# Performance work log

Hardware: AMD Instinct MI355X
Metric: run time of the kernel (lower is better)

Reference implementation:

```python
import jax, jax.numpy as jnp
import numpy as np

N, LAT, H, R, L = 384, 64, 128, 16, 3
CUTOFF = 12.0
COORD_INIT_SCALE = 0.001


def setup_inputs() -> dict:
    key = jax.random.key(0)
    ks = jax.random.split(key, 12)
    def w(k, shape, fan):
        return jax.random.normal(k, shape, jnp.float32) / np.float32(np.sqrt(fan))
    return {
        "z": jax.random.normal(ks[0], (N, LAT), jnp.float32),
        # spread anchors so the radius graph is non-trivially sparse
        "anchor_coords": jax.random.normal(ks[1], (N, 3), jnp.float32) * 10.0,
        "proj_W": w(ks[2], (LAT, H), LAT),
        "proj_b": jnp.zeros((H,), jnp.float32),
        "eW1": w(ks[3], (L, 2 * H + R, H), 2 * H + R),
        "eb1": jnp.zeros((L, H), jnp.float32),
        "eW2": w(ks[4], (L, H, H), H),
        "eb2": jnp.zeros((L, H), jnp.float32),
        "nW1": w(ks[5], (L, 2 * H, H), 2 * H),
        "nb1": jnp.zeros((L, H), jnp.float32),
        "nW2": w(ks[6], (L, H, H), H),
        "nb2": jnp.zeros((L, H), jnp.float32),
        "cW1": w(ks[7], (L, H, H), H),
        "cb1": jnp.zeros((L, H), jnp.float32),
        # coord head scaled by coord_update_init_scale for stable coordinate updates
        "cW2": w(ks[8], (L, H, 1), H) * COORD_INIT_SCALE,
    }


def _rbf(d):
    # Gaussian radial basis expansion over [0, cutoff]
    mu = jnp.linspace(0.0, CUTOFF, R, dtype=d.dtype)            # (R,)
    gamma = jnp.asarray((R / CUTOFF) ** 2, d.dtype)
    return jnp.exp(-gamma * (d[..., None] - mu) ** 2)           # (..., R)


def reference(z, anchor_coords, proj_W, proj_b, eW1, eb1, eW2, eb2,
              nW1, nb1, nW2, nb2, cW1, cb1, cW2):
    silu = jax.nn.silu
    n = z.shape[0]
    h = z @ proj_W + proj_b                                      # (N, H)
    x = anchor_coords - anchor_coords.mean(0, keepdims=True)     # (N, 3)

    idx = jnp.arange(n)
    seq_mask = jnp.abs(idx[:, None] - idx[None, :]) == 1         # sequential edges
    eye = jnp.eye(n, dtype=bool)

    for l in range(L):
        # rebuild radius graph from current coords (dense jit-safe mask)
        diff = x[:, None, :] - x[None, :, :]                     # (N, N, 3) x_i - x_j
        d2 = jnp.sum(diff * diff, axis=-1)                       # (N, N)
        mask = ((d2 < CUTOFF ** 2) & ~eye) | seq_mask            # (N, N) bool
        maskf = mask.astype(h.dtype)
        d = jnp.sqrt(jnp.where(mask, d2, 1.0)) * maskf           # NaN-safe sqrt
        e = _rbf(d)                                              # (N, N, R)

        hi = jnp.broadcast_to(h[:, None, :], (n, n, H))          # receiver
        hj = jnp.broadcast_to(h[None, :, :], (n, n, H))          # sender
        m = silu(jnp.concatenate([hi, hj, e], -1) @ eW1[l] + eb1[l])
        m = silu(m @ eW2[l] + eb2[l]) * maskf[..., None]         # (N, N, H) messages

        agg = m.sum(1)                                           # scatter-add at receiver
        h = h + silu(jnp.concatenate([h, agg], -1) @ nW1[l] + nb1[l]) @ nW2[l] + nb2[l]

        w = (silu(m @ cW1[l] + cb1[l]) @ cW2[l]) * maskf[..., None]  # (N, N, 1)
        x = x + jnp.sum(diff * w, axis=1)                        # equivariant coord update
    return x
```

## Files before the change

### kernel.cpp

```cpp
#include <hip/hip_runtime.h>
#include <hip/hip_bf16.h>

#define NN 384
#define CUTOFF2 144.0f
#define GAMMA 1.7777778f

#define PK_L 26624
#define PK_WE 8192
#define PK_W2 10240
#define PK_C1 18432

#define STG_F32 1152
#define SCRATCH_B (8*STG_F32*4)
#define PERSIST_OFF (PK_L*4 + SCRATCH_B)
#define K_SMEM (PERSIST_OFF + 15408)

#define O_H    9216
#define O_A    205824
#define O_XA   0
#define O_XB   4608
#define O_HBF0 599040
#define O_HBF1 697344
#define O_MEAN 3076112
#define O_PK   3076160

typedef __bf16 bf16x8 __attribute__((ext_vector_type(8)));
typedef float f32x4 __attribute__((ext_vector_type(4)));

union ER { struct { float dx, dy, dz; unsigned j; } e; uint4 u4; };

__device__ __forceinline__ unsigned short f2bf(float f){
  unsigned u = __float_as_uint(f);
  return (unsigned short)((u + 0x7fffu + ((u >> 16) & 1u)) >> 16);
}
__device__ __forceinline__ unsigned pk2(float a, float b){
  return ((unsigned)f2bf(b) << 16) | f2bf(a);
}
__device__ __forceinline__ float silu(float x){ return x / (1.0f + __expf(-x)); }

__device__ __forceinline__ void scan_rows(
    int row, int rowsel, int t256, bool v, const float* __restrict__ x,
    uint4* sEr, int* pCnt){
  int* scnt = &pCnt[rowsel];
  if (t256 == 0) *scnt = 0;
  __syncthreads();
  if (v) {
    float xi0 = x[row*3], xi1 = x[row*3+1], xi2 = x[row*3+2];
    for (int j = t256; j < 384; j += 256) {
      float d0 = xi0-x[j*3], d1 = xi1-x[j*3+1], d2 = xi2-x[j*3+2];
      float dd = d0*d0 + d1*d1 + d2*d2;
      bool msk = ((dd < CUTOFF2) && (j != row)) || (j == row-1) || (j == row+1);
      if (msk) {
        int ss = atomicAdd(scnt, 1);
        ER er; er.e.dx = d0; er.e.dy = d1; er.e.dz = d2; er.e.j = (unsigned)j;
        sEr[rowsel*384 + ss] = er.u4;
      }
    }
  }
  __syncthreads();
  if (v) {
    int cnt = *scnt;
    int p = (32 - (cnt & 31)) & 31;
    if (t256 < p) {
      ER er; er.e.dx = 0.f; er.e.dy = 0.f; er.e.dz = 0.f; er.e.j = (unsigned)row;
      sEr[rowsel*384 + cnt + t256] = er.u4;
    }
  }
}

#define TRANSFORM(VA, VB, FA, FB)                                              \
  _Pragma("unroll")                                                            \
  for (int c = 0; c < 4; ++c) {                                                \
    _Pragma("unroll")                                                          \
    for (int tl = 0; tl < 2; ++tl) {                                           \
      int t = 2*c + tl;                                                        \
      _Pragma("unroll")                                                        \
      for (int r = 0; r < 4; ++r) {                                            \
        stg[(quad*4 + r)*36 + tl*16 + col0] = VA[t][r];                        \
        stg[(16 + quad*4 + r)*36 + tl*16 + col0] = VB[t][r];                   \
      }                                                                        \
    }                                                                          \
    float4 lo = *(const float4*)(stg + col0*36 + quad*8);                      \
    float4 hi = *(const float4*)(stg + col0*36 + quad*8 + 4);                  \
    FA[c].u = make_uint4(pk2(lo.x,lo.y), pk2(lo.z,lo.w),                       \
                         pk2(hi.x,hi.y), pk2(hi.z,hi.w));                      \
    float4 lo2 = *(const float4*)(stg + (16 + col0)*36 + quad*8);              \
    float4 hi2 = *(const float4*)(stg + (16 + col0)*36 + quad*8 + 4);          \
    FB[c].u = make_uint4(pk2(lo2.x,lo2.y), pk2(lo2.z,lo2.w),                   \
                         pk2(hi2.x,hi2.y), pk2(hi2.z,hi2.w));                  \
  }

__device__ __forceinline__ void edge_phase(
    const unsigned short* __restrict__ hbf,
    const unsigned* smem, float* scratch,
    const float* pSa, float* pSg, float* pDx, const int* pCnt, const uint4* sEr,
    const float* __restrict__ eb2g, const float* __restrict__ cb1g,
    const float* __restrict__ cw2g, int valid1){
  const int tid = threadIdx.x, q = tid & 63, s = tid >> 6;
  const int col0 = q & 15, quad = q >> 4;
  float eb2v[8], cb1v[8], cw2v[8];
  #pragma unroll
  for (int t = 0; t < 8; ++t) {
    int c = t*16 + col0;
    eb2v[t] = eb2g[c]; cb1v[t] = cb1g[c]; cw2v[t] = cw2g[c];
  }
  float* stg = scratch + s*STG_F32;
  const f32x4 z4 = {0.f, 0.f, 0.f, 0.f};
  union U8 { uint4 u; bf16x8 v; };

  const int nu0 = (pCnt[0] + 31) >> 5;
  const int nu1 = valid1 ? ((pCnt[1] + 31) >> 5) : 0;
  const int nu = nu0 + nu1;

  for (int k = s; k < nu; k += 8) {
    const int rs = (k < nu0) ? 0 : 1;
    const int ub = (k < nu0) ? k : k - nu0;
    int nvalid = pCnt[rs] - ub*32; if (nvalid > 32) nvalid = 32;
    float Aval[8];
    #pragma unroll
    for (int t = 0; t < 8; ++t) Aval[t] = pSa[rs*128 + t*16 + col0];
    ER e0, e1;
    e0.u4 = sEr[rs*384 + ub*32 + col0];
    e1.u4 = sEr[rs*384 + ub*32 + 16 + col0];
    const int j0 = (int)e0.e.j, j1 = (int)e1.e.j;
    const float d0x = e0.e.dx, d0y = e0.e.dy, d0z = e0.e.dz;
    const float d1x = e1.e.dx, d1y = e1.e.dy, d1z = e1.e.dz;
    const float dd0 = sqrtf(d0x*d0x + d0y*d0y + d0z*d0z);
    const float dd1 = sqrtf(d1x*d1x + d1y*d1y + d1z*d1z);

    U8 ha0[4], ha1[4];
    #pragma unroll
    for (int c = 0; c < 4; ++c) {
      ha0[c].u = *(const uint4*)(hbf + j0*128 + c*32 + quad*8);
      ha1[c].u = *(const uint4*)(hbf + j1*128 + c*32 + quad*8);
    }

    U8 cve0, cve1;
    if (q < 32) {
      #pragma unroll
      for (int tp = 0; tp < 4; ++tp) {
        float k0 = (float)(quad*8 + 2*tp);
        float t00 = dd0 - 0.8f*k0, t01 = dd0 - 0.8f*(k0+1.f);
        float t10 = dd1 - 0.8f*k0, t11 = dd1 - 0.8f*(k0+1.f);
        (&cve0.u.x)[tp] = pk2(__expf(-GAMMA*t00*t00), __expf(-GAMMA*t01*t01));
        (&cve1.u.x)[tp] = pk2(__expf(-GAMMA*t10*t10), __expf(-GAMMA*t11*t11));
      }
    } else { cve0.u = make_uint4(0,0,0,0); cve1.u = make_uint4(0,0,0,0); }

    f32x4 acc0[8], acc1[8];
    #pragma unroll
    for (int t = 0; t < 8; ++t) { acc0[t] = z4; acc1[t] = z4; }
    #pragma unroll
    for (int t = 0; t < 8; ++t) {
      #pragma unroll
      for (int c = 0; c < 4; ++c) {
        bf16x8 w = *(const bf16x8*)(smem + ((t*4 + c)*64 + q)*4);
        acc0[t] = __builtin_amdgcn_mfma_f32_16x16x32_bf16(ha0[c].v, w, acc0[t], 0, 0, 0);
        acc1[t] = __builtin_amdgcn_mfma_f32_16x16x32_bf16(ha1[c].v, w, acc1[t], 0, 0, 0);
      }
      bf16x8 we = *(const bf16x8*)(smem + PK_WE + (t*64 + q)*4);
      acc0[t] = __builtin_amdgcn_mfma_f32_16x16x32_bf16(cve0.v, we, acc0[t], 0, 0, 0);
      acc1[t] = __builtin_amdgcn_mfma_f32_16x16x32_bf16(cve1.v, we, acc1[t], 0, 0, 0);
    }
    #pragma unroll
    for (int t = 0; t < 8; ++t)
      #pragma unroll
      for (int r = 0; r < 4; ++r) {
        acc0[t][r] = silu(acc0[t][r] + Aval[t]);
        acc1[t][r] = silu(acc1[t][r] + Aval[t]);
      }

    U8 a20[4], a21[4];
    TRANSFORM(acc0, acc1, a20, a21);

    f32x4 m0[8], m1v[8];
    #pragma unroll
    for (int t = 0; t < 8; ++t) { m0[t] = z4; m1v[t] = z4; }
    #pragma unroll
    for (int t = 0; t < 8; ++t)
      #pragma unroll
      for (int c = 0; c < 4; ++c) {
        bf16x8 w = *(const bf16x8*)(smem + PK_W2 + ((t*4 + c)*64 + q)*4);
        m0[t] = __builtin_amdgcn_mfma_f32_16x16x32_bf16(a20[c].v, w, m0[t], 0, 0, 0);
        m1v[t] = __builtin_amdgcn_mfma_f32_16x16x32_bf16(a21[c].v, w, m1v[t], 0, 0, 0);
      }
    #pragma unroll
    for (int t = 0; t < 8; ++t) {
      float cs = 0.f;
      #pragma unroll
      for (int r = 0; r < 4; ++r) {
        m0[t][r] = silu(m0[t][r] + eb2v[t]);
        m1v[t][r] = silu(m1v[t][r] + eb2v[t]);
        if (quad*4 + r < nvalid) cs += m0[t][r];
        if (16 + quad*4 + r < nvalid) cs += m1v[t][r];
      }
      cs += __shfl_xor(cs, 16); cs += __shfl_xor(cs, 32);
      if (q < 16) atomicAdd(&pSg[rs*128 + t*16 + q], cs);
    }

    U8 a30[4], a31[4];
    TRANSFORM(m0, m1v, a30, a31);

    f32x4 c30[8], c31[8];
    #pragma unroll
    for (int t = 0; t < 8; ++t) { c30[t] = z4; c31[t] = z4; }
    #pragma unroll
    for (int t = 0; t < 8; ++t)
      #pragma unroll
      for (int c = 0; c < 4; ++c) {
        bf16x8 w = *(const bf16x8*)(smem + PK_C1 + ((t*4 + c)*64 + q)*4);
        c30[t] = __builtin_amdgcn_mfma_f32_16x16x32_bf16(a30[c].v, w, c30[t], 0, 0, 0);
        c31[t] = __builtin_amdgcn_mfma_f32_16x16x32_bf16(a31[c].v, w, c31[t], 0, 0, 0);
      }
    float p0[4], p1[4];
    #pragma unroll
    for (int r = 0; r < 4; ++r) {
      float pa = 0.f, pb = 0.f;
      #pragma unroll
      for (int t = 0; t < 8; ++t) {
        pa += silu(c30[t][r] + cb1v[t]) * cw2v[t];
        pb += silu(c31[t][r] + cb1v[t]) * cw2v[t];
      }
      if (quad*4 + r >= nvalid) pa = 0.f;
      if (16 + quad*4 + r >= nvalid) pb = 0.f;
      p0[r] = pa; p1[r] = pb;
    }
    #pragma unroll
    for (int r = 0; r < 4; ++r)
      #pragma unroll
      for (int off = 1; off < 16; off <<= 1) {
        p0[r] += __shfl_xor(p0[r], off);
        p1[r] += __shfl_xor(p1[r], off);
      }
    float dx0 = 0.f, dx1 = 0.f, dx2 = 0.f;
    #pragma unroll
    for (int r = 0; r < 4; ++r) {
      int el = quad*4 + r;
      float s0 = __shfl(d0x, el), s1 = __shfl(d0y, el), s2 = __shfl(d0z, el);
      if (col0 == 0) { dx0 += p0[r]*s0; dx1 += p0[r]*s1; dx2 += p0[r]*s2; }
      float u0 = __shfl(d1x, el), u1 = __shfl(d1y, el), u2 = __shfl(d1z, el);
      if (col0 == 0) { dx0 += p1[r]*u0; dx1 += p1[r]*u1; dx2 += p1[r]*u2; }
    }
    dx0 += __shfl_xor(dx0, 16); dx0 += __shfl_xor(dx0, 32);
    dx1 += __shfl_xor(dx1, 16); dx1 += __shfl_xor(dx1, 32);
    dx2 += __shfl_xor(dx2, 16); dx2 += __shfl_xor(dx2, 32);
    if (q == 0) {
      atomicAdd(&pDx[rs*4 + 0], dx0);
      atomicAdd(&pDx[rs*4 + 1], dx1);
      atomicAdd(&pDx[rs*4 + 2], dx2);
    }
  }
}

__device__ __forceinline__ void node_phase(
    const float* __restrict__ nW1l, const float* __restrict__ nb1l,
    const float* __restrict__ nW2l, const float* __restrict__ nb2l,
    const float* __restrict__ eW1n, const float* __restrict__ eb1n,
    unsigned short* __restrict__ hbf_out,
    float* __restrict__ hg, float* __restrict__ Ag,
    float* pSh, float* pSa, const float* pSg,
    float* scratch, int rowsel, int half, int o, int row, bool v){
  float* sb = scratch + rowsel*768;
  float* st = sb; float* part = sb + 128;

  float aa = 0.f;
  if (v) {
    const float* src = half ? (pSg + rowsel*128) : (pSh + rowsel*128);
    const float* wb  = nW1l + half*128*128;
    float a0=0,a1=0,a2=0,a3=0;
    #pragma unroll 16
    for (int k = 0; k < 128; k += 4) {
      a0 += src[k]   * wb[k*128 + o];
      a1 += src[k+1] * wb[(k+1)*128 + o];
      a2 += src[k+2] * wb[(k+2)*128 + o];
      a3 += src[k+3] * wb[(k+3)*128 + o];
    }
    aa = (a0+a1)+(a2+a3);
    if (half) part[o] = aa;
  }
  __syncthreads();
  if (v && !half) st[o] = silu(nb1l[o] + aa + part[o]);
  __syncthreads();
  float bb = 0.f;
  if (v) {
    int k0 = half*64;
    float b0=0,b1=0,b2=0,b3=0;
    #pragma unroll 16
    for (int k = k0; k < k0+64; k += 4) {
      b0 += st[k]   * nW2l[k*128 + o];
      b1 += st[k+1] * nW2l[(k+1)*128 + o];
      b2 += st[k+2] * nW2l[(k+2)*128 + o];
      b3 += st[k+3] * nW2l[(k+3)*128 + o];
    }
    bb = (b0+b1)+(b2+b3);
    if (half) part[o] = bb;
  }
  __syncthreads();
  if (v && !half) {
    float hn = pSh[rowsel*128 + o] + nb2l[o] + bb + part[o];
    pSh[rowsel*128 + o] = hn;
    hg[row*128 + o] = hn;
    hbf_out[row*128 + o] = f2bf(hn);
  }
  __syncthreads();
  float cc = 0.f;
  if (v) {
    const float* shn = pSh + rowsel*128;
    int k0 = half*64;
    float c0=0,c1=0,c2=0,c3=0;
    #pragma unroll 16
    for (int k = k0; k < k0+64; k += 4) {
      c0 += shn[k]   * eW1n[k*128 + o];
      c1 += shn[k+1] * eW1n[(k+1)*128 + o];
      c2 += shn[k+2] * eW1n[(k+2)*128 + o];
      c3 += shn[k+3] * eW1n[(k+3)*128 + o];
    }
    cc = (c0+c1)+(c2+c3);
    if (half) part[o] = cc;
  }
  __syncthreads();
  if (v && !half) Ag[row*128 + o] = eb1n[o] + cc + part[o];
}

__global__ __launch_bounds__(512) void k_init(
    const float* __restrict__ eW1, const float* __restrict__ eW2,
    const float* __restrict__ cW1, unsigned* __restrict__ pk,
    const float* __restrict__ anchor, const float* __restrict__ z,
    const float* __restrict__ pW, const float* __restrict__ pbias,
    const float* __restrict__ eb1, float* __restrict__ h,
    unsigned short* __restrict__ hbf, float* __restrict__ A,
    float* __restrict__ meanw){
  __shared__ float sb2[2*768];
  __shared__ float ssum[3];
  const int b = blockIdx.x, tid = threadIdx.x;
  const int rowsel = tid >> 8, half = (tid >> 7) & 1, o = tid & 127;
  {
    int t = b*512 + tid;
    if (t < 3*PK_L) {
      int layer = t / PK_L, r = t % PK_L;
      const float* src; int fr; int isWe = 0;
      if (r < PK_WE)        { fr = r;          src = eW1 + (layer*272 + 128)*128; }
      else if (r < PK_W2)   { fr = r - PK_WE;  src = eW1 + (layer*272 + 256)*128; isWe = 1; }
      else if (r < PK_C1)   { fr = r - PK_W2;  src = eW2 + layer*128*128; }
      else                  { fr = r - PK_C1;  src = cW1 + layer*128*128; }
      int tp = fr & 3, ll = (fr >> 2) & 63, nc = fr >> 8;
      int n, k;
      if (!isWe) { n = nc >> 2; int c = nc & 3; k = c*32 + ((ll>>4)<<3) + 2*tp; }
      else       { n = nc;                      k = ((ll>>4)<<3) + 2*tp; }
      int nn2 = n*16 + (ll & 15);
      float w0, w1;
      if (isWe) { w0 = (k < 16)   ? src[k*128+nn2]     : 0.f;
                  w1 = (k+1 < 16) ? src[(k+1)*128+nn2] : 0.f; }
      else      { w0 = src[k*128+nn2]; w1 = src[(k+1)*128+nn2]; }
      pk[t] = ((unsigned)f2bf(w1) << 16) | f2bf(w0);
    }
  }
  if (b == 0) {
    if (tid < 3) ssum[tid] = 0.f;
    __syncthreads();
    if (tid < 384) {
      atomicAdd(&ssum[0], anchor[tid*3]);
      atomicAdd(&ssum[1], anchor[tid*3+1]);
      atomicAdd(&ssum[2], anchor[tid*3+2]);
    }
    __syncthreads();
    if (tid < 3) meanw[tid] = ssum[tid]*(1.f/384.f);
  }
  const int row = b + 256*rowsel;
  const bool v = row < NN;
  float* sb = sb2 + rowsel*768;
  float* sh = sb; float* part = sb + 512; float* sz = sb + 640;
  if (v && half == 0 && o < 64) sz[o] = z[row*64 + o];
  __syncthreads();
  float pp = 0.f;
  if (v) {
    int k0 = half*32;
    float p0=0,p1=0,p2=0,p3=0;
    #pragma unroll 8
    for (int k = k0; k < k0+32; k += 4) {
      p0 += sz[k]   * pW[k*128 + o];
      p1 += sz[k+1] * pW[(k+1)*128 + o];
      p2 += sz[k+2] * pW[(k+2)*128 + o];
      p3 += sz[k+3] * pW[(k+3)*128 + o];
    }
    pp = (p0+p1)+(p2+p3);
    if (half) part[o] = pp;
  }
  __syncthreads();
  if (v && !half) {
    float hh = pbias[o] + pp + part[o];
    h[row*128 + o] = hh; sh[o] = hh;
    hbf[row*128 + o] = f2bf(hh);
  }
  __syncthreads();
  float cc = 0.f;
  if (v) {
    int k0 = half*64;
    float c0=0,c1=0,c2=0,c3=0;
    #pragma unroll 16
    for (int k = k0; k < k0+64; k += 4) {
      c0 += sh[k]   * eW1[k*128 + o];
      c1 += sh[k+1] * eW1[(k+1)*128 + o];
      c2 += sh[k+2] * eW1[(k+2)*128 + o];
      c3 += sh[k+3] * eW1[(k+3)*128 + o];
    }
    cc = (c0+c1)+(c2+c3);
    if (half) part[o] = cc;
  }
  __syncthreads();
  if (v && !half) A[row*128 + o] = eb1[o] + cc + part[o];
}

__global__ __launch_bounds__(512, 1) void k_layer(
    const unsigned* __restrict__ pkl,
    const float* __restrict__ x_src, float* __restrict__ x_dst,
    const unsigned short* __restrict__ hbf_in, unsigned short* __restrict__ hbf_out,
    float* __restrict__ h, float* __restrict__ A,
    const float* __restrict__ eb2l, const float* __restrict__ cb1l,
    const float* __restrict__ cw2l,
    const float* __restrict__ nW1l, const float* __restrict__ nb1l,
    const float* __restrict__ nW2l, const float* __restrict__ nb2l,
    const float* __restrict__ eW1n, const float* __restrict__ eb1n,
    const float* __restrict__ meanp, int do_node){
  extern __shared__ unsigned smem[];
  const int b = blockIdx.x, tid = threadIdx.x;
  const int rowsel = tid >> 8, half = (tid >> 7) & 1, o = tid & 127, t256 = tid & 255;
  const int row = b + 256*rowsel;
  const bool v = row < NN;
  float* scratch = (float*)(smem + PK_L);
  char* pb8 = (char*)smem + PERSIST_OFF;
  float* pSh = (float*)pb8;
  float* pSa = pSh + 256;
  float* pSg = pSa + 256;
  float* pDx = pSg + 256;
  int*   pCnt = (int*)(pDx + 8);
  uint4* sEr = (uint4*)(pb8 + 3120);

  for (int idx = tid; idx < PK_L/4; idx += 512)
    ((uint4*)smem)[idx] = ((const uint4*)pkl)[idx];
  if (tid < 256) {
    int rr = b + 256*(tid >> 7);
    if (rr < NN) {
      pSh[tid] = h[rr*128 + (tid & 127)];
      pSa[tid] = A[rr*128 + (tid & 127)];
    }
    pSg[tid] = 0.f;
  } else if (tid < 264) pDx[tid - 256] = 0.f;
  scan_rows(row, rowsel, t256, v, x_src, sEr, pCnt);
  __syncthreads();
  edge_phase(hbf_in, smem, scratch, pSa, pSg, pDx, pCnt, sEr,
             eb2l, cb1l, cw2l, b < 128);
  __syncthreads();
  if (v && half == 0 && o < 3) {
    float xn = x_src[row*3 + o] + pDx[rowsel*4 + o];
    x_dst[row*3 + o] = meanp ? (xn - meanp[o]) : xn;
  }
  if (do_node)
    node_phase(nW1l, nb1l, nW2l, nb2l, eW1n, eb1n, hbf_out, h, A,
               pSh, pSa, pSg, scratch, rowsel, half, o, row, v);
}

extern "C" void kernel_launch(void* const* d_in, const int* in_sizes, int n_in,
                              void* d_out, int out_size, void* d_ws, size_t ws_size,
                              hipStream_t stream){
  const float* z      = (const float*)d_in[0];
  const float* anchor = (const float*)d_in[1];
  const float* projW  = (const float*)d_in[2];
  const float* projb  = (const float*)d_in[3];
  const float* eW1    = (const float*)d_in[4];
  const float* eb1    = (const float*)d_in[5];
  const float* eW2    = (const float*)d_in[6];
  const float* eb2    = (const float*)d_in[7];
  const float* nW1    = (const float*)d_in[8];
  const float* nb1    = (const float*)d_in[9];
  const float* nW2    = (const float*)d_in[10];
  const float* nb2    = (const float*)d_in[11];
  const float* cW1    = (const float*)d_in[12];
  const float* cb1    = (const float*)d_in[13];
  const float* cW2    = (const float*)d_in[14];
  float* out = (float*)d_out;

  char* w = (char*)d_ws;
  float* xA  = (float*)(w + O_XA);
  float* xB  = (float*)(w + O_XB);
  float* h   = (float*)(w + O_H);
  float* A   = (float*)(w + O_A);
  unsigned short* hbf0 = (unsigned short*)(w + O_HBF0);
  unsigned short* hbf1 = (unsigned short*)(w + O_HBF1);
  float* meanw = (float*)(w + O_MEAN);
  unsigned* pk = (unsigned*)(w + O_PK);

  hipFuncSetAttribute((const void*)k_layer, hipFuncAttributeMaxDynamicSharedMemorySize, K_SMEM);

  k_init<<<256, 512, 0, stream>>>(eW1, eW2, cW1, pk, anchor, z, projW, projb,
                                  eb1, h, hbf0, A, meanw);
  k_layer<<<256, 512, K_SMEM, stream>>>(pk, anchor, xB, hbf0, hbf1, h, A,
      eb2, cb1, cW2,
      nW1, nb1, nW2, nb2, eW1 + 272*128, eb1 + 128,
      (const float*)nullptr, 1);
  k_layer<<<256, 512, K_SMEM, stream>>>(pk + PK_L, xB, xA, hbf1, hbf0, h, A,
      eb2 + 128, cb1 + 128, cW2 + 128,
      nW1 + 256*128, nb1 + 128, nW2 + 128*128, nb2 + 128,
      eW1 + 2*272*128, eb1 + 256,
      (const float*)nullptr, 1);
  k_layer<<<256, 512, K_SMEM, stream>>>(pk + 2*PK_L, xA, out, hbf0, hbf1, h, A,
      eb2 + 256, cb1 + 256, cW2 + 256,
      nW1, nb1, nW2, nb2, eW1, eb1,
      meanw, 0);
}
```

Measured before the change: 177.9 us.

## Fuse init into layer-0 kernel and fold projection into sender weights

Merges the init kernel into a new layer-0 kernel, removing one launch and the round-trip of h/A through global memory. For layer 0 the sender half of eW1 is premultiplied by projW in each block, so the edge MLP reads the 64-wide z directly and needs only 2 MFMA k-chunks instead of 4. Each block redundantly computes the 64x128 folded weight and packs layer-0 weights into LDS, which adds per-block setup work and rounding differences from bf16 z.

```diff
diff --git a/kernel.cpp b/kernel.cpp
--- a/kernel.cpp
+++ b/kernel.cpp
@@ -90,8 +90,9 @@
                          pk2(hi2.x,hi2.y), pk2(hi2.z,hi2.w));                  \
   }
 
+template<int IS_L0>
 __device__ __forceinline__ void edge_phase(
-    const unsigned short* __restrict__ hbf,
+    const unsigned short* __restrict__ hbf, const float* __restrict__ zg,
     const unsigned* smem, float* scratch,
     const float* pSa, float* pSg, float* pDx, const int* pCnt, const uint4* sEr,
     const float* __restrict__ eb2g, const float* __restrict__ cb1g,
@@ -129,10 +130,24 @@
     const float dd1 = sqrtf(d1x*d1x + d1y*d1y + d1z*d1z);
 
     U8 ha0[4], ha1[4];
-    #pragma unroll
-    for (int c = 0; c < 4; ++c) {
-      ha0[c].u = *(const uint4*)(hbf + j0*128 + c*32 + quad*8);
-      ha1[c].u = *(const uint4*)(hbf + j1*128 + c*32 + quad*8);
+    if (IS_L0) {
+      #pragma unroll
+      for (int c = 0; c < 2; ++c) {
+        const float* zr0 = zg + j0*64 + c*32 + quad*8;
+        const float* zr1 = zg + j1*64 + c*32 + quad*8;
+        float4 a0 = *(const float4*)zr0, a1 = *(const float4*)(zr0 + 4);
+        ha0[c].u = make_uint4(pk2(a0.x,a0.y), pk2(a0.z,a0.w),
+                              pk2(a1.x,a1.y), pk2(a1.z,a1.w));
+        float4 b0 = *(const float4*)zr1, b1 = *(const float4*)(zr1 + 4);
+        ha1[c].u = make_uint4(pk2(b0.x,b0.y), pk2(b0.z,b0.w),
+                              pk2(b1.x,b1.y), pk2(b1.z,b1.w));
+      }
+    } else {
+      #pragma unroll
+      for (int c = 0; c < 4; ++c) {
+        ha0[c].u = *(const uint4*)(hbf + j0*128 + c*32 + quad*8);
+        ha1[c].u = *(const uint4*)(hbf + j1*128 + c*32 + quad*8);
+      }
     }
 
     U8 cve0, cve1;
@@ -153,7 +168,7 @@
     #pragma unroll
     for (int t = 0; t < 8; ++t) {
       #pragma unroll
-      for (int c = 0; c < 4; ++c) {
+      for (int c = 0; c < (IS_L0 ? 2 : 4); ++c) {
         bf16x8 w = *(const bf16x8*)(smem + ((t*4 + c)*64 + q)*4);
         acc0[t] = __builtin_amdgcn_mfma_f32_16x16x32_bf16(ha0[c].v, w, acc0[t], 0, 0, 0);
         acc1[t] = __builtin_amdgcn_mfma_f32_16x16x32_bf16(ha1[c].v, w, acc1[t], 0, 0, 0);
@@ -322,22 +337,37 @@
   if (v && !half) Ag[row*128 + o] = eb1n[o] + cc + part[o];
 }
 
-__global__ __launch_bounds__(512) void k_init(
-    const float* __restrict__ eW1, const float* __restrict__ eW2,
-    const float* __restrict__ cW1, unsigned* __restrict__ pk,
-    const float* __restrict__ anchor, const float* __restrict__ z,
-    const float* __restrict__ pW, const float* __restrict__ pbias,
-    const float* __restrict__ eb1, float* __restrict__ h,
-    unsigned short* __restrict__ hbf, float* __restrict__ A,
-    float* __restrict__ meanw){
-  __shared__ float sb2[2*768];
-  __shared__ float ssum[3];
+__global__ __launch_bounds__(512, 1) void k_layer0(
+    const float* __restrict__ z, const float* __restrict__ anchor,
+    const float* __restrict__ projW, const float* __restrict__ projb,
+    const float* __restrict__ eW1, const float* __restrict__ eb1,
+    const float* __restrict__ eW2, const float* __restrict__ eb2,
+    const float* __restrict__ nW1, const float* __restrict__ nb1,
+    const float* __restrict__ nW2, const float* __restrict__ nb2,
+    const float* __restrict__ cW1, const float* __restrict__ cb1,
+    const float* __restrict__ cW2,
+    float* __restrict__ x_dst, unsigned short* __restrict__ hbf_out,
+    float* __restrict__ h, float* __restrict__ A,
+    float* __restrict__ meanw, unsigned* __restrict__ pk){
+  extern __shared__ unsigned smem[];
   const int b = blockIdx.x, tid = threadIdx.x;
-  const int rowsel = tid >> 8, half = (tid >> 7) & 1, o = tid & 127;
+  const int rowsel = tid >> 8, half = (tid >> 7) & 1, o = tid & 127, t256 = tid & 255;
+  const int row = b + 256*rowsel;
+  const bool v = row < NN;
+  float* scratch = (float*)(smem + PK_L);
+  char* pb8 = (char*)smem + PERSIST_OFF;
+  float* pSh = (float*)pb8;
+  float* pSa = pSh + 256;
+  float* pSg = pSa + 256;
+  float* pDx = pSg + 256;
+  int*   pCnt = (int*)(pDx + 8);
+  uint4* sEr = (uint4*)(pb8 + 3120);
+  const float* W1bg = eW1 + 128*128;
+
   {
     int t = b*512 + tid;
-    if (t < 3*PK_L) {
-      int layer = t / PK_L, r = t % PK_L;
+    if (t < 2*PK_L) {
+      int layer = 1 + t / PK_L, r = t % PK_L;
       const float* src; int fr; int isWe = 0;
       if (r < PK_WE)        { fr = r;          src = eW1 + (layer*272 + 128)*128; }
       else if (r < PK_W2)   { fr = r - PK_WE;  src = eW1 + (layer*272 + 256)*128; isWe = 1; }
@@ -356,6 +386,7 @@
     }
   }
   if (b == 0) {
+    float* ssum = scratch + 8448;
     if (tid < 3) ssum[tid] = 0.f;
     __syncthreads();
     if (tid < 384) {
@@ -366,49 +397,123 @@
     __syncthreads();
     if (tid < 3) meanw[tid] = ssum[tid]*(1.f/384.f);
   }
-  const int row = b + 256*rowsel;
-  const bool v = row < NN;
-  float* sb = sb2 + rowsel*768;
-  float* sh = sb; float* part = sb + 512; float* sz = sb + 640;
-  if (v && half == 0 && o < 64) sz[o] = z[row*64 + o];
-  __syncthreads();
-  float pp = 0.f;
-  if (v) {
-    int k0 = half*32;
-    float p0=0,p1=0,p2=0,p3=0;
-    #pragma unroll 8
-    for (int k = k0; k < k0+32; k += 4) {
-      p0 += sz[k]   * pW[k*128 + o];
-      p1 += sz[k+1] * pW[(k+1)*128 + o];
-      p2 += sz[k+2] * pW[(k+2)*128 + o];
-      p3 += sz[k+3] * pW[(k+3)*128 + o];
-    }
-    pp = (p0+p1)+(p2+p3);
-    if (half) part[o] = pp;
-  }
-  __syncthreads();
-  if (v && !half) {
-    float hh = pbias[o] + pp + part[o];
-    h[row*128 + o] = hh; sh[o] = hh;
-    hbf[row*128 + o] = f2bf(hh);
-  }
-  __syncthreads();
-  float cc = 0.f;
-  if (v) {
-    int k0 = half*64;
-    float c0=0,c1=0,c2=0,c3=0;
-    #pragma unroll 16
-    for (int k = k0; k < k0+64; k += 4) {
-      c0 += sh[k]   * eW1[k*128 + o];
-      c1 += sh[k+1] * eW1[(k+1)*128 + o];
-      c2 += sh[k+2] * eW1[(k+2)*128 + o];
-      c3 += sh[k+3] * eW1[(k+3)*128 + o];
-    }
-    cc = (c0+c1)+(c2+c3);
-    if (half) part[o] = cc;
-  }
-  __syncthreads();
-  if (v && !half) A[row*128 + o] = eb1[o] + cc + part[o];
+  {
+    float* sPW = scratch;
+    for (int idx = tid; idx < 64*128; idx += 512) {
+      int k = idx >> 7, m = idx & 127;
+      sPW[k*132 + m] = projW[idx];
+    }
+    for (int idx = tid; idx < 2048; idx += 512) smem[PK_WE + idx] = 0;
+  }
+  __syncthreads();
+  {
+    const float* sPW = scratch;
+    int n = tid & 127, g = tid >> 7;
+    float acc[16];
+    #pragma unroll
+    for (int i = 0; i < 16; ++i) acc[i] = 0.f;
+    for (int m = 0; m < 128; m += 4) {
+      float4 wv;
+      wv.x = W1bg[m*128 + n];     wv.y = W1bg[(m+1)*128 + n];
+      wv.z = W1bg[(m+2)*128 + n]; wv.w = W1bg[(m+3)*128 + n];
+      #pragma unroll
+      for (int i = 0; i < 16; ++i) {
+        const float4 pv = *(const float4*)(sPW + (g*16 + i)*132 + m);
+        acc[i] += pv.x*wv.x + pv.y*wv.y + pv.z*wv.z + pv.w*wv.w;
+      }
+    }
+    #pragma unroll
+    for (int p = 0; p < 8; ++p) {
+      int k0 = g*16 + 2*p;
+      int c = k0 >> 5, kin = k0 & 31;
+      int hi3 = kin >> 3, tp = (kin & 7) >> 1;
+      int l = hi3*16 + (n & 15);
+      int nc = (n >> 4)*4 + c;
+      smem[tp + 4*l + 256*nc] = pk2(acc[2*p], acc[2*p+1]);
+    }
+    {
+      const float* src = eW1 + 256*128;
+      for (int sidx = tid; sidx < 16*128; sidx += 512) {
+        int k = sidx >> 7, nn = sidx & 127;
+        unsigned short hv = f2bf(src[sidx]);
+        int hi = k >> 3, tp = (k & 7) >> 1, hf = k & 1;
+        int l = hi*16 + (nn & 15), nc = nn >> 4;
+        int fr = PK_WE + tp + 4*l + 256*nc;
+        ((unsigned short*)smem)[fr*2 + hf] = hv;
+      }
+    }
+    const float* s2 = eW2; const float* s3 = cW1;
+    for (int pass = 0; pass < 2; ++pass) {
+      const float* src = pass ? s3 : s2;
+      int base = pass ? PK_C1 : PK_W2;
+      for (int sidx = tid; sidx < 128*128; sidx += 512) {
+        int k = sidx >> 7, nn = sidx & 127;
+        unsigned short hv = f2bf(src[sidx]);
+        int c = k >> 5, kin = k & 31;
+        int hi = kin >> 3, tp = (kin & 7) >> 1, hf = kin & 1;
+        int l = hi*16 + (nn & 15), nc = (nn >> 4)*4 + c;
+        int fr = base + tp + 4*l + 256*nc;
+        ((unsigned short*)smem)[fr*2 + hf] = hv;
+      }
+    }
+    if (tid < 128) {
+      float sum = 0.f;
+      for (int m = 0; m < 128; ++m) sum += projb[m]*W1bg[m*128 + tid];
+      scratch[8576 + tid] = sum;
+    }
+  }
+  __syncthreads();
+  {
+    float* sb = scratch + rowsel*768;
+    float* part = sb + 512; float* sz = sb + 640;
+    if (v && half == 0 && o < 64) sz[o] = z[row*64 + o];
+    __syncthreads();
+    float pp = 0.f;
+    if (v) {
+      int k0 = half*32;
+      float p0=0,p1=0,p2=0,p3=0;
+      #pragma unroll 8
+      for (int k = k0; k < k0+32; k += 4) {
+        p0 += sz[k]   * projW[k*128 + o];
+        p1 += sz[k+1] * projW[(k+1)*128 + o];
+        p2 += sz[k+2] * projW[(k+2)*128 + o];
+        p3 += sz[k+3] * projW[(k+3)*128 + o];
+      }
+      pp = (p0+p1)+(p2+p3);
+      if (half) part[o] = pp;
+    }
+    __syncthreads();
+    if (v && !half) pSh[rowsel*128 + o] = projb[o] + pp + part[o];
+    __syncthreads();
+    float cc = 0.f;
+    if (v) {
+      const float* sh = pSh + rowsel*128;
+      int k0 = half*64;
+      float c0=0,c1=0,c2=0,c3=0;
+      #pragma unroll 16
+      for (int k = k0; k < k0+64; k += 4) {
+        c0 += sh[k]   * eW1[k*128 + o];
+        c1 += sh[k+1] * eW1[(k+1)*128 + o];
+        c2 += sh[k+2] * eW1[(k+2)*128 + o];
+        c3 += sh[k+3] * eW1[(k+3)*128 + o];
+      }
+      cc = (c0+c1)+(c2+c3);
+      if (half) part[o] = cc;
+    }
+    __syncthreads();
+    if (v && !half) pSa[rowsel*128 + o] = eb1[o] + cc + part[o] + scratch[8576 + o];
+  }
+  if (tid < 256) pSg[tid] = 0.f;
+  else if (tid < 264) pDx[tid - 256] = 0.f;
+  scan_rows(row, rowsel, t256, v, anchor, sEr, pCnt);
+  __syncthreads();
+  edge_phase<1>(nullptr, z, smem, scratch, pSa, pSg, pDx, pCnt, sEr,
+                eb2, cb1, cW2, b < 128);
+  __syncthreads();
+  if (v && half == 0 && o < 3)
+    x_dst[row*3 + o] = anchor[row*3 + o] + pDx[rowsel*4 + o];
+  node_phase(nW1, nb1, nW2, nb2, eW1 + 272*128, eb1 + 128, hbf_out, h, A,
+             pSh, pSa, pSg, scratch, rowsel, half, o, row, v);
 }
 
 __global__ __launch_bounds__(512, 1) void k_layer(
@@ -448,8 +553,8 @@
   } else if (tid < 264) pDx[tid - 256] = 0.f;
   scan_rows(row, rowsel, t256, v, x_src, sEr, pCnt);
   __syncthreads();
-  edge_phase(hbf_in, smem, scratch, pSa, pSg, pDx, pCnt, sEr,
-             eb2l, cb1l, cw2l, b < 128);
+  edge_phase<0>(hbf_in, nullptr, smem, scratch, pSa, pSg, pDx, pCnt, sEr,
+                eb2l, cb1l, cw2l, b < 128);
   __syncthreads();
   if (v && half == 0 && o < 3) {
     float xn = x_src[row*3 + o] + pDx[rowsel*4 + o];
@@ -490,20 +595,18 @@
   float* meanw = (float*)(w + O_MEAN);
   unsigned* pk = (unsigned*)(w + O_PK);
 
-  hipFuncSetAttribute((const void*)k_layer, hipFuncAttributeMaxDynamicSharedMemorySize, K_SMEM);
-
-  k_init<<<256, 512, 0, stream>>>(eW1, eW2, cW1, pk, anchor, z, projW, projb,
-                                  eb1, h, hbf0, A, meanw);
-  k_layer<<<256, 512, K_SMEM, stream>>>(pk, anchor, xB, hbf0, hbf1, h, A,
-      eb2, cb1, cW2,
-      nW1, nb1, nW2, nb2, eW1 + 272*128, eb1 + 128,
-      (const float*)nullptr, 1);
-  k_layer<<<256, 512, K_SMEM, stream>>>(pk + PK_L, xB, xA, hbf1, hbf0, h, A,
+  hipFuncSetAttribute((const void*)k_layer0, hipFuncAttributeMaxDynamicSharedMemorySize, K_SMEM);
+  hipFuncSetAttribute((const void*)k_layer,  hipFuncAttributeMaxDynamicSharedMemorySize, K_SMEM);
+
+  k_layer0<<<256, 512, K_SMEM, stream>>>(z, anchor, projW, projb, eW1, eb1,
+      eW2, eb2, nW1, nb1, nW2, nb2, cW1, cb1, cW2,
+      xB, hbf0, h, A, meanw, pk);
+  k_layer<<<256, 512, K_SMEM, stream>>>(pk, xB, xA, hbf0, hbf1, h, A,
       eb2 + 128, cb1 + 128, cW2 + 128,
       nW1 + 256*128, nb1 + 128, nW2 + 128*128, nb2 + 128,
       eW1 + 2*272*128, eb1 + 256,
       (const float*)nullptr, 1);
-  k_layer<<<256, 512, K_SMEM, stream>>>(pk + 2*PK_L, xA, out, hbf0, hbf1, h, A,
+  k_layer<<<256, 512, K_SMEM, stream>>>(pk + PK_L, xA, out, hbf1, hbf0, h, A,
       eb2 + 256, cb1 + 256, cW2 + 256,
       nW1, nb1, nW2, nb2, eW1, eb1,
       meanw, 0);
```

Measured after the change: 189.1 us. +6.3%, slower.

## Use one row per 256-thread block and read packed weights from global

Applied to the files above, without the earlier changes.

The layer kernel now launches one block of 256 threads per node row (384 blocks) instead of 256 blocks of 512 threads, each handling up to two rows. The weight pack is no longer staged into shared memory; the MFMA B operands are loaded straight from global memory (through cache), and shared memory drops to small static arrays so two blocks can fit per CU. This removes the per-block weight copy and the row imbalance of the old two-rows-per-block mapping. In exchange every MFMA weight fetch now goes through the global/L2 path rather than LDS.

```diff
diff --git a/kernel.cpp b/kernel.cpp
--- a/kernel.cpp
+++ b/kernel.cpp
@@ -11,9 +11,6 @@
 #define PK_C1 18432
 
 #define STG_F32 1152
-#define SCRATCH_B (8*STG_F32*4)
-#define PERSIST_OFF (PK_L*4 + SCRATCH_B)
-#define K_SMEM (PERSIST_OFF + 15408)
 
 #define O_H    9216
 #define O_A    205824
@@ -38,32 +35,30 @@
 }
 __device__ __forceinline__ float silu(float x){ return x / (1.0f + __expf(-x)); }
 
-__device__ __forceinline__ void scan_rows(
-    int row, int rowsel, int t256, bool v, const float* __restrict__ x,
-    uint4* sEr, int* pCnt){
-  int* scnt = &pCnt[rowsel];
-  if (t256 == 0) *scnt = 0;
-  __syncthreads();
-  if (v) {
+__device__ __forceinline__ void scan_row1(
+    int row, int tid, const float* __restrict__ x, uint4* sEr, int* pCnt){
+  if (tid == 0) pCnt[0] = 0;
+  __syncthreads();
+  {
     float xi0 = x[row*3], xi1 = x[row*3+1], xi2 = x[row*3+2];
-    for (int j = t256; j < 384; j += 256) {
+    for (int j = tid; j < 384; j += 256) {
       float d0 = xi0-x[j*3], d1 = xi1-x[j*3+1], d2 = xi2-x[j*3+2];
       float dd = d0*d0 + d1*d1 + d2*d2;
       bool msk = ((dd < CUTOFF2) && (j != row)) || (j == row-1) || (j == row+1);
       if (msk) {
-        int ss = atomicAdd(scnt, 1);
+        int ss = atomicAdd(pCnt, 1);
         ER er; er.e.dx = d0; er.e.dy = d1; er.e.dz = d2; er.e.j = (unsigned)j;
-        sEr[rowsel*384 + ss] = er.u4;
-      }
-    }
-  }
-  __syncthreads();
-  if (v) {
-    int cnt = *scnt;
+        sEr[ss] = er.u4;
+      }
+    }
+  }
+  __syncthreads();
+  {
+    int cnt = pCnt[0];
     int p = (32 - (cnt & 31)) & 31;
-    if (t256 < p) {
+    if (tid < p) {
       ER er; er.e.dx = 0.f; er.e.dy = 0.f; er.e.dz = 0.f; er.e.j = (unsigned)row;
-      sEr[rowsel*384 + cnt + t256] = er.u4;
+      sEr[cnt + tid] = er.u4;
     }
   }
 }
@@ -91,11 +86,11 @@
   }
 
 __device__ __forceinline__ void edge_phase(
-    const unsigned short* __restrict__ hbf,
-    const unsigned* smem, float* scratch,
-    const float* pSa, float* pSg, float* pDx, const int* pCnt, const uint4* sEr,
+    const unsigned short* __restrict__ hbf, const unsigned* __restrict__ pkl,
+    float* scratch, const float* pSa, float* pSg, float* pDx,
+    int cnt, const uint4* sEr,
     const float* __restrict__ eb2g, const float* __restrict__ cb1g,
-    const float* __restrict__ cw2g, int valid1){
+    const float* __restrict__ cw2g){
   const int tid = threadIdx.x, q = tid & 63, s = tid >> 6;
   const int col0 = q & 15, quad = q >> 4;
   float eb2v[8], cb1v[8], cw2v[8];
@@ -108,20 +103,16 @@
   const f32x4 z4 = {0.f, 0.f, 0.f, 0.f};
   union U8 { uint4 u; bf16x8 v; };
 
-  const int nu0 = (pCnt[0] + 31) >> 5;
-  const int nu1 = valid1 ? ((pCnt[1] + 31) >> 5) : 0;
-  const int nu = nu0 + nu1;
-
-  for (int k = s; k < nu; k += 8) {
-    const int rs = (k < nu0) ? 0 : 1;
-    const int ub = (k < nu0) ? k : k - nu0;
-    int nvalid = pCnt[rs] - ub*32; if (nvalid > 32) nvalid = 32;
+  const int nu = (cnt + 31) >> 5;
+
+  for (int k = s; k < nu; k += 4) {
+    int nvalid = cnt - k*32; if (nvalid > 32) nvalid = 32;
     float Aval[8];
     #pragma unroll
-    for (int t = 0; t < 8; ++t) Aval[t] = pSa[rs*128 + t*16 + col0];
+    for (int t = 0; t < 8; ++t) Aval[t] = pSa[t*16 + col0];
     ER e0, e1;
-    e0.u4 = sEr[rs*384 + ub*32 + col0];
-    e1.u4 = sEr[rs*384 + ub*32 + 16 + col0];
+    e0.u4 = sEr[k*32 + col0];
+    e1.u4 = sEr[k*32 + 16 + col0];
     const int j0 = (int)e0.e.j, j1 = (int)e1.e.j;
     const float d0x = e0.e.dx, d0y = e0.e.dy, d0z = e0.e.dz;
     const float d1x = e1.e.dx, d1y = e1.e.dy, d1z = e1.e.dz;
@@ -154,11 +145,11 @@
     for (int t = 0; t < 8; ++t) {
       #pragma unroll
       for (int c = 0; c < 4; ++c) {
-        bf16x8 w = *(const bf16x8*)(smem + ((t*4 + c)*64 + q)*4);
+        bf16x8 w = *(const bf16x8*)(pkl + ((t*4 + c)*64 + q)*4);
         acc0[t] = __builtin_amdgcn_mfma_f32_16x16x32_bf16(ha0[c].v, w, acc0[t], 0, 0, 0);
         acc1[t] = __builtin_amdgcn_mfma_f32_16x16x32_bf16(ha1[c].v, w, acc1[t], 0, 0, 0);
       }
-      bf16x8 we = *(const bf16x8*)(smem + PK_WE + (t*64 + q)*4);
+      bf16x8 we = *(const bf16x8*)(pkl + PK_WE + (t*64 + q)*4);
       acc0[t] = __builtin_amdgcn_mfma_f32_16x16x32_bf16(cve0.v, we, acc0[t], 0, 0, 0);
       acc1[t] = __builtin_amdgcn_mfma_f32_16x16x32_bf16(cve1.v, we, acc1[t], 0, 0, 0);
     }
@@ -180,7 +171,7 @@
     for (int t = 0; t < 8; ++t)
       #pragma unroll
       for (int c = 0; c < 4; ++c) {
-        bf16x8 w = *(const bf16x8*)(smem + PK_W2 + ((t*4 + c)*64 + q)*4);
+        bf16x8 w = *(const bf16x8*)(pkl + PK_W2 + ((t*4 + c)*64 + q)*4);
         m0[t] = __builtin_amdgcn_mfma_f32_16x16x32_bf16(a20[c].v, w, m0[t], 0, 0, 0);
         m1v[t] = __builtin_amdgcn_mfma_f32_16x16x32_bf16(a21[c].v, w, m1v[t], 0, 0, 0);
       }
@@ -195,7 +186,7 @@
         if (16 + quad*4 + r < nvalid) cs += m1v[t][r];
       }
       cs += __shfl_xor(cs, 16); cs += __shfl_xor(cs, 32);
-      if (q < 16) atomicAdd(&pSg[rs*128 + t*16 + q], cs);
+      if (q < 16) atomicAdd(&pSg[t*16 + q], cs);
     }
 
     U8 a30[4], a31[4];
@@ -208,7 +199,7 @@
     for (int t = 0; t < 8; ++t)
       #pragma unroll
       for (int c = 0; c < 4; ++c) {
-        bf16x8 w = *(const bf16x8*)(smem + PK_C1 + ((t*4 + c)*64 + q)*4);
+        bf16x8 w = *(const bf16x8*)(pkl + PK_C1 + ((t*4 + c)*64 + q)*4);
         c30[t] = __builtin_amdgcn_mfma_f32_16x16x32_bf16(a30[c].v, w, c30[t], 0, 0, 0);
         c31[t] = __builtin_amdgcn_mfma_f32_16x16x32_bf16(a31[c].v, w, c31[t], 0, 0, 0);
       }
@@ -245,9 +236,9 @@
     dx1 += __shfl_xor(dx1, 16); dx1 += __shfl_xor(dx1, 32);
     dx2 += __shfl_xor(dx2, 16); dx2 += __shfl_xor(dx2, 32);
     if (q == 0) {
-      atomicAdd(&pDx[rs*4 + 0], dx0);
-      atomicAdd(&pDx[rs*4 + 1], dx1);
-      atomicAdd(&pDx[rs*4 + 2], dx2);
+      atomicAdd(&pDx[0], dx0);
+      atomicAdd(&pDx[1], dx1);
+      atomicAdd(&pDx[2], dx2);
     }
   }
 }
@@ -259,13 +250,12 @@
     unsigned short* __restrict__ hbf_out,
     float* __restrict__ hg, float* __restrict__ Ag,
     float* pSh, float* pSa, const float* pSg,
-    float* scratch, int rowsel, int half, int o, int row, bool v){
-  float* sb = scratch + rowsel*768;
-  float* st = sb; float* part = sb + 128;
+    float* scratch, int half, int o, int row){
+  float* st = scratch; float* part = scratch + 128;
 
   float aa = 0.f;
-  if (v) {
-    const float* src = half ? (pSg + rowsel*128) : (pSh + rowsel*128);
+  {
+    const float* src = half ? pSg : pSh;
     const float* wb  = nW1l + half*128*128;
     float a0=0,a1=0,a2=0,a3=0;
     #pragma unroll 16
@@ -279,10 +269,10 @@
     if (half) part[o] = aa;
   }
   __syncthreads();
-  if (v && !half) st[o] = silu(nb1l[o] + aa + part[o]);
+  if (!half) st[o] = silu(nb1l[o] + aa + part[o]);
   __syncthreads();
   float bb = 0.f;
-  if (v) {
+  {
     int k0 = half*64;
     float b0=0,b1=0,b2=0,b3=0;
     #pragma unroll 16
@@ -296,30 +286,29 @@
     if (half) part[o] = bb;
   }
   __syncthreads();
-  if (v && !half) {
-    float hn = pSh[rowsel*128 + o] + nb2l[o] + bb + part[o];
-    pSh[rowsel*128 + o] = hn;
+  if (!half) {
+    float hn = pSh[o] + nb2l[o] + bb + part[o];
+    pSh[o] = hn;
     hg[row*128 + o] = hn;
     hbf_out[row*128 + o] = f2bf(hn);
   }
   __syncthreads();
   float cc = 0.f;
-  if (v) {
-    const float* shn = pSh + rowsel*128;
+  {
     int k0 = half*64;
     float c0=0,c1=0,c2=0,c3=0;
     #pragma unroll 16
     for (int k = k0; k < k0+64; k += 4) {
-      c0 += shn[k]   * eW1n[k*128 + o];
-      c1 += shn[k+1] * eW1n[(k+1)*128 + o];
-      c2 += shn[k+2] * eW1n[(k+2)*128 + o];
-      c3 += shn[k+3] * eW1n[(k+3)*128 + o];
+      c0 += pSh[k]   * eW1n[k*128 + o];
+      c1 += pSh[k+1] * eW1n[(k+1)*128 + o];
+      c2 += pSh[k+2] * eW1n[(k+2)*128 + o];
+      c3 += pSh[k+3] * eW1n[(k+3)*128 + o];
     }
     cc = (c0+c1)+(c2+c3);
     if (half) part[o] = cc;
   }
   __syncthreads();
-  if (v && !half) Ag[row*128 + o] = eb1n[o] + cc + part[o];
+  if (!half) Ag[row*128 + o] = eb1n[o] + cc + part[o];
 }
 
 __global__ __launch_bounds__(512) void k_init(
@@ -411,7 +400,7 @@
   if (v && !half) A[row*128 + o] = eb1[o] + cc + part[o];
 }
 
-__global__ __launch_bounds__(512, 1) void k_layer(
+__global__ __launch_bounds__(256, 2) void k_layer(
     const unsigned* __restrict__ pkl,
     const float* __restrict__ x_src, float* __restrict__ x_dst,
     const unsigned short* __restrict__ hbf_in, unsigned short* __restrict__ hbf_out,
@@ -422,42 +411,27 @@
     const float* __restrict__ nW2l, const float* __restrict__ nb2l,
     const float* __restrict__ eW1n, const float* __restrict__ eb1n,
     const float* __restrict__ meanp, int do_node){
-  extern __shared__ unsigned smem[];
-  const int b = blockIdx.x, tid = threadIdx.x;
-  const int rowsel = tid >> 8, half = (tid >> 7) & 1, o = tid & 127, t256 = tid & 255;
-  const int row = b + 256*rowsel;
-  const bool v = row < NN;
-  float* scratch = (float*)(smem + PK_L);
-  char* pb8 = (char*)smem + PERSIST_OFF;
-  float* pSh = (float*)pb8;
-  float* pSa = pSh + 256;
-  float* pSg = pSa + 256;
-  float* pDx = pSg + 256;
-  int*   pCnt = (int*)(pDx + 8);
-  uint4* sEr = (uint4*)(pb8 + 3120);
-
-  for (int idx = tid; idx < PK_L/4; idx += 512)
-    ((uint4*)smem)[idx] = ((const uint4*)pkl)[idx];
-  if (tid < 256) {
-    int rr = b + 256*(tid >> 7);
-    if (rr < NN) {
-      pSh[tid] = h[rr*128 + (tid & 127)];
-      pSa[tid] = A[rr*128 + (tid & 127)];
-    }
-    pSg[tid] = 0.f;
-  } else if (tid < 264) pDx[tid - 256] = 0.f;
-  scan_rows(row, rowsel, t256, v, x_src, sEr, pCnt);
-  __syncthreads();
-  edge_phase(hbf_in, smem, scratch, pSa, pSg, pDx, pCnt, sEr,
-             eb2l, cb1l, cw2l, b < 128);
-  __syncthreads();
-  if (v && half == 0 && o < 3) {
-    float xn = x_src[row*3 + o] + pDx[rowsel*4 + o];
-    x_dst[row*3 + o] = meanp ? (xn - meanp[o]) : xn;
+  __shared__ float scratch[4*STG_F32];
+  __shared__ float pSh[128], pSa[128], pSg[128], pDx[4];
+  __shared__ int pCnt[4];
+  __shared__ uint4 sEr[384];
+  const int row = blockIdx.x, tid = threadIdx.x;
+  const int half = tid >> 7, o = tid & 127;
+
+  if (tid < 128) { pSh[tid] = h[row*128 + tid]; pSg[tid] = 0.f; }
+  else           { pSa[o] = A[row*128 + o]; if (o < 4) pDx[o] = 0.f; }
+  scan_row1(row, tid, x_src, sEr, pCnt);
+  __syncthreads();
+  edge_phase(hbf_in, pkl, scratch, pSa, pSg, pDx, pCnt[0], sEr,
+             eb2l, cb1l, cw2l);
+  __syncthreads();
+  if (tid < 3) {
+    float xn = x_src[row*3 + tid] + pDx[tid];
+    x_dst[row*3 + tid] = meanp ? (xn - meanp[tid]) : xn;
   }
   if (do_node)
     node_phase(nW1l, nb1l, nW2l, nb2l, eW1n, eb1n, hbf_out, h, A,
-               pSh, pSa, pSg, scratch, rowsel, half, o, row, v);
+               pSh, pSa, pSg, scratch, half, o, row);
 }
 
 extern "C" void kernel_launch(void* const* d_in, const int* in_sizes, int n_in,
@@ -490,20 +464,18 @@
   float* meanw = (float*)(w + O_MEAN);
   unsigned* pk = (unsigned*)(w + O_PK);
 
-  hipFuncSetAttribute((const void*)k_layer, hipFuncAttributeMaxDynamicSharedMemorySize, K_SMEM);
-
   k_init<<<256, 512, 0, stream>>>(eW1, eW2, cW1, pk, anchor, z, projW, projb,
                                   eb1, h, hbf0, A, meanw);
-  k_layer<<<256, 512, K_SMEM, stream>>>(pk, anchor, xB, hbf0, hbf1, h, A,
+  k_layer<<<384, 256, 0, stream>>>(pk, anchor, xB, hbf0, hbf1, h, A,
       eb2, cb1, cW2,
       nW1, nb1, nW2, nb2, eW1 + 272*128, eb1 + 128,
       (const float*)nullptr, 1);
-  k_layer<<<256, 512, K_SMEM, stream>>>(pk + PK_L, xB, xA, hbf1, hbf0, h, A,
+  k_layer<<<384, 256, 0, stream>>>(pk + PK_L, xB, xA, hbf1, hbf0, h, A,
       eb2 + 128, cb1 + 128, cW2 + 128,
       nW1 + 256*128, nb1 + 128, nW2 + 128*128, nb2 + 128,
       eW1 + 2*272*128, eb1 + 256,
       (const float*)nullptr, 1);
-  k_layer<<<256, 512, K_SMEM, stream>>>(pk + 2*PK_L, xA, out, hbf0, hbf1, h, A,
+  k_layer<<<384, 256, 0, stream>>>(pk + 2*PK_L, xA, out, hbf0, hbf1, h, A,
       eb2 + 256, cb1 + 256, cW2 + 256,
       nW1, nb1, nW2, nb2, eW1, eb1,
       meanw, 0);
```

Result: slower. 294.0 us (+65.3%).
